# Kernel tuning notes

Measured on AMD Instinct MI355X. Metric: run time of the kernel, lower is better.

## Reference

```python
import jax, jax.numpy as jnp
import numpy as np

R = 4          # corr_radius
SLOPE = 0.1    # leaky relu negative slope


def _conv(x, w, b, pad):
    y = jax.lax.conv_general_dilated(
        x, w, window_strides=(1, 1), padding=[(pad, pad), (pad, pad)],
        dimension_numbers=("NCHW", "OIHW", "NCHW"))
    return y + b[None, :, None, None]


def _correlation(x1, x2):
    # Fused windowed cost volume: cv[b, i*(2R+1)+j, h, w] = mean_c x1[b,c,h,w] * x2[b,c,h+i-R,w+j-R]
    B, C, H, W = x1.shape
    x2p = jnp.pad(x2, ((0, 0), (0, 0), (R, R), (R, R)))
    cv = jnp.stack(
        [jnp.mean(x1 * jax.lax.dynamic_slice(x2p, (0, 0, i, j), (B, C, H, W)), axis=1)
         for i in range(2 * R + 1) for j in range(2 * R + 1)], axis=1)
    return cv  # (B, (2R+1)^2, H, W)


def setup_inputs() -> dict:
    key = jax.random.key(0)
    ks = jax.random.split(key, 20)
    B, H, W = 2, 256, 256
    pyr = 24
    inp = {
        "feat0": jax.random.normal(ks[0], (B, 2 * pyr, H, W), jnp.float32),
        "feat1": jax.random.normal(ks[1], (B, 2 * pyr, H, W), jnp.float32),
        "last_feat": jax.random.normal(ks[2], (B, 64, H, W), jnp.float32),
        "last_flow": jax.random.normal(ks[3], (B, 4, H, W), jnp.float32),
    }
    in_ch = (2 * R + 1) ** 2 + 2 * (2 * pyr) + 64 + 4  # 245
    dims = [(160, in_ch, 1), (128, 160, 3), (112, 128, 3), (96, 112, 3), (64, 96, 3), (4, 64, 3)]
    for n, (co, ci, k) in enumerate(dims, 1):
        scale = 1.0 / np.sqrt(ci * k * k)
        inp[f"w{n}"] = jax.random.normal(ks[4 + 2 * n], (co, ci, k, k), jnp.float32) * scale
        inp[f"b{n}"] = jnp.zeros((co,), jnp.float32)
    return inp


def reference(feat0, feat1, last_feat, last_flow,
              w1, b1, w2, b2, w3, b3, w4, b4, w5, b5, w6, b6):
    lrelu = lambda x: jax.nn.leaky_relu(x, SLOPE)
    volume = lrelu(_correlation(feat0, feat1))
    feat = jnp.concatenate([volume, feat0, feat1, last_feat, last_flow], axis=1)
    x = lrelu(_conv(feat, w1, b1, 0))   # 1x1 conv
    x = lrelu(_conv(x, w2, b2, 1))
    x = lrelu(_conv(x, w3, b3, 1))
    x = lrelu(_conv(x, w4, b4, 1))
    x = lrelu(_conv(x, w5, b5, 1))
    flow = _conv(x, w6, b6, 1)          # final ConvBlock, act=None
    return flow, x
```

## Files before the change

kernel.cpp:

```cpp
#include <hip/hip_runtime.h>
#include <cstdint>
#include <cstddef>


using short8 = __attribute__((ext_vector_type(8))) short;
using f32x4  = __attribute__((ext_vector_type(4))) float;
typedef unsigned short u16;

__device__ __forceinline__ u16 rne_bf16(float f) {
  unsigned u = __float_as_uint(f);
  u += 0x7FFFu + ((u >> 16) & 1u);
  return (u16)(u >> 16);
}

__device__ __forceinline__ void mfma16(const short8& a, const short8& b, f32x4& c) {
  asm("v_mfma_f32_16x16x32_bf16 %0, %1, %2, %0" : "+v"(c) : "v"(a), "v"(b));
}

__device__ __forceinline__ unsigned pk_f16(float a, float b) {
  unsigned r;
  asm("v_cvt_pkrtz_f16_f32 %0, %1, %2" : "=v"(r) : "v"(a), "v"(b));
  return r;
}

__device__ __forceinline__ void dot2(float& acc, unsigned a, unsigned b) {
  asm("v_dot2_f32_f16 %0, %1, %2, %0" : "+v"(acc) : "v"(a), "v"(b));
}

__device__ __forceinline__ void gload16(const void* g, void* l) {
  __builtin_amdgcn_global_load_lds(
      (const __attribute__((address_space(1))) unsigned int*)g,
      (__attribute__((address_space(3))) unsigned int*)l, 16, 0, 0);
}

__global__ __launch_bounds__(256) void prep1_kernel(const float* __restrict__ w1,
                                                    u16* __restrict__ w1p) {
  int idx = blockIdx.x * 256 + threadIdx.x;
  int co = idx >> 8, cip = idx & 255;
  float v = 0.f;
  if (co < 160 && cip < 245) {
    int ci = (cip < 164) ? (cip + 81) : (cip - 164);
    v = w1[co * 245 + ci];
  }
  w1p[idx] = rne_bf16(v);
}

template<int CO, int CIr, int BM, int APLN, int CIP>
__global__ __launch_bounds__(256) void prep3s_kernel(const float* __restrict__ w,
                                                     u16* __restrict__ wp) {
  int idx = blockIdx.x * 256 + threadIdx.x;
  int ci = idx % CIP; int rest = idx / CIP;
  int row = rest % APLN; int dyp = rest / APLN;
  int dx = row / BM, co = row % BM;
  float v = 0.f;
  if (dx < 3 && co < CO && ci < CIr)
    v = w[(co * CIr + ci) * 9 + dyp * 3 + dx];
  wp[idx] = rne_bf16(v);
}

template<int CO, int CI, int COP, int CIP>
__global__ __launch_bounds__(256) void prep3_kernel(const float* __restrict__ w,
                                                    u16* __restrict__ wp) {
  int idx = blockIdx.x * 256 + threadIdx.x;
  int ci = idx % CIP; int rest = idx / CIP;
  int co = rest % COP; int tap = rest / COP;
  float v = 0.f;
  if (co < CO && ci < CI) v = w[(co * CI + ci) * 9 + tap];
  wp[idx] = rne_bf16(v);
}

__global__ __launch_bounds__(256) void prep_bias_kernel(const float* __restrict__ b1,
    const float* __restrict__ b2, const float* __restrict__ b3,
    const float* __restrict__ b4, const float* __restrict__ b5,
    float* __restrict__ bp, u16* __restrict__ zbuf) {
  int i = blockIdx.x * 256 + threadIdx.x;
  if (i < 128) zbuf[i] = 0;
  float v = 0.f;
  if (i < 160) v = b1[i];
  else if (i < 288) v = b2[i - 160];
  else if (i < 416) { int c = i - 288; v = (c < 112) ? b3[c] : 0.f; }
  else if (i < 512) v = b4[i - 416];
  else if (i < 576) v = b5[i - 512];
  else return;
  bp[i] = v;
}

template<int NDY>
__device__ __forceinline__ void corr_compute(const uint2* __restrict__ win_s,
                                             const unsigned* __restrict__ f0p,
                                             float* __restrict__ cv,
                                             int row, int col, int dy0) {
#pragma unroll
  for (int d = 0; d < NDY; ++d) {
    const int r = row + dy0 + d;
#pragma unroll
    for (int cpp = 0; cpp < 6; ++cpp) {
      const uint2* base = win_s + (cpp * 10 + r) * 72 + col;
#pragma unroll
      for (int dx = 0; dx < 9; ++dx) {
        const uint2 v = base[dx];
        dot2(cv[d * 9 + dx], v.x, f0p[2 * cpp]);
        dot2(cv[d * 9 + dx], v.y, f0p[2 * cpp + 1]);
      }
    }
  }
}

__global__ __launch_bounds__(256) void corr2_kernel(const float* __restrict__ f0,
                                                    const float* __restrict__ f1,
                                                    u16* __restrict__ X1) {
  __shared__ uint2 win_s[4320];
  const int bid = blockIdx.x;
  const int swz = (bid & 7) * 128 + (bid >> 3);
  const int b = swz >> 9, rest = swz & 511;
  const int hp = rest >> 2, ct = rest & 3;
  const int h0 = hp << 1, w0 = ct << 6;
  const int tid = threadIdx.x, lane = tid & 63, wv = tid >> 6;
  const int half = wv >> 1, row = wv & 1, col = lane;

  float cv[45];
#pragma unroll
  for (int t = 0; t < 45; ++t) cv[t] = 0.f;

#pragma unroll 1
  for (int cc = 0; cc < 2; ++cc) {
    if (cc) __syncthreads();
    unsigned f0p[12];
    {
      const float* p0 = f0 + (((size_t)(b * 48 + cc * 24)) << 16)
                           + ((h0 + row) << 8) + (w0 + col);
#pragma unroll
      for (int j = 0; j < 12; ++j)
        f0p[j] = pk_f16(p0[(2 * j) << 16], p0[(2 * j + 1) << 16]);
    }
#pragma unroll 1
    for (int i = tid; i < 4320; i += 256) {
      const int c = i % 72;
      const int q = i / 72;
      const int r = q % 10;
      const int cpp = q / 10;
      const int hin = h0 + r - 4, win = w0 + c - 4;
      float v0 = 0.f, v1 = 0.f, v2 = 0.f, v3 = 0.f;
      if ((unsigned)hin < 256u && (unsigned)win < 256u) {
        const float* p = f1 + (((size_t)(b * 48 + cc * 24 + cpp * 4)) << 16)
                            + (hin << 8) + win;
        v0 = p[0]; v1 = p[1 << 16]; v2 = p[2 << 16]; v3 = p[3 << 16];
      }
      win_s[i] = make_uint2(pk_f16(v0, v1), pk_f16(v2, v3));
    }
    __syncthreads();
    if (half == 0) corr_compute<4>(win_s, f0p, cv, row, col, 0);
    else           corr_compute<5>(win_s, f0p, cv, row, col, 4);
  }

  const size_t pix = ((size_t)b << 16) + ((size_t)(h0 + row) << 8) + (w0 + col);
  u16* dst = X1 + pix * 256;
  const float sc = 1.0f / 48.0f;
  if (half == 0) {
#pragma unroll
    for (int qq = 0; qq < 9; ++qq) {
      u16 e[4];
#pragma unroll
      for (int j = 0; j < 4; ++j) {
        float v = cv[qq * 4 + j] * sc;
        v = v > 0.f ? v : 0.1f * v;
        e[j] = rne_bf16(v);
      }
      uint2 u;
      u.x = (unsigned)e[0] | ((unsigned)e[1] << 16);
      u.y = (unsigned)e[2] | ((unsigned)e[3] << 16);
      *(uint2*)(dst + 164 + qq * 4) = u;
    }
  } else {
#pragma unroll
    for (int qq = 0; qq < 14; ++qq) {
      u16 e[4];
#pragma unroll
      for (int j = 0; j < 4; ++j) {
        int t = qq * 4 + j;
        float v = 0.f;
        if (t < 45) {
          v = cv[t] * sc;
          v = v > 0.f ? v : 0.1f * v;
        }
        e[j] = rne_bf16(v);
      }
      uint2 u;
      u.x = (unsigned)e[0] | ((unsigned)e[1] << 16);
      u.y = (unsigned)e[2] | ((unsigned)e[3] << 16);
      *(uint2*)(dst + 200 + qq * 4) = u;
    }
  }
}

__global__ __launch_bounds__(256) void concat_kernel(const float* __restrict__ f0,
                                                     const float* __restrict__ f1,
                                                     const float* __restrict__ lf,
                                                     const float* __restrict__ lfl,
                                                     u16* __restrict__ X1) {
  __shared__ float s[16][68];
  const int t = threadIdx.x;
  const size_t px0 = (size_t)blockIdx.x * 64;
  const int b = blockIdx.x >> 10;
  const int hw0 = (blockIdx.x & 1023) * 64;

#pragma unroll 1
  for (int cc = 0; cc < 11; ++cc) {
    __syncthreads();
    {
      int px = t & 63, cg = t >> 6;
#pragma unroll
      for (int r = 0; r < 4; ++r) {
        int cl = cg * 4 + r;
        int c = cc * 16 + cl;
        int hw = hw0 + px;
        float v = 0.f;
        if (c < 48)       v = f0[(((size_t)(b * 48 + c)) << 16) + hw];
        else if (c < 96)  v = f1[(((size_t)(b * 48 + (c - 48))) << 16) + hw];
        else if (c < 160) v = lf[(((size_t)(b * 64 + (c - 96))) << 16) + hw];
        else if (c < 164) v = lfl[(((size_t)(b * 4 + (c - 160))) << 16) + hw];
        s[cl][px] = v;
      }
    }
    __syncthreads();
    {
      int px = t >> 2, g = t & 3;
      int cbase = cc * 16 + g * 4;
      if (cbase < 164) {
        ushort4 u;
        u.x = rne_bf16(s[g * 4 + 0][px]);
        u.y = rne_bf16(s[g * 4 + 1][px]);
        u.z = rne_bf16(s[g * 4 + 2][px]);
        u.w = rne_bf16(s[g * 4 + 3][px]);
        *(ushort4*)(X1 + (px0 + px) * 256 + cbase) = u;
      }
    }
  }
}

template<int CI, int BM, int APLN, int KS, int OSTRIDE, bool LRELU, bool OBF, int COF32>
__global__ __launch_bounds__(256) void convs_kernel(const u16* __restrict__ Xin,
    const u16* __restrict__ Wp, const float* __restrict__ bias,
    const u16* __restrict__ zbuf, u16* __restrict__ Xout,
    float* __restrict__ outF) {
  constexpr int NCH = CI / 32;
  constexpr int NDX = (KS == 3) ? 3 : 1;
  constexpr int AROUNDS = APLN / 64;
  constexpr int BROUNDS = (KS == 3) ? 3 : 2;
  constexpr int MF = BM / 32;
  constexpr int AELEMS = AROUNDS * 2048;
  constexpr int BPXMAX = (KS == 3) ? 132 : 128;
  __shared__ u16 lds[(AROUNDS + BROUNDS) * 2048];

  const int tid = threadIdx.x;
  const int lane = tid & 63, wv = tid >> 6;
  const int wm = wv >> 1, wn = wv & 1;
  const int bid = blockIdx.x;
  const int swz = (bid & 7) * 128 + (bid >> 3);
  const int bi = swz >> 9;
  const int h = (swz >> 1) & 255;
  const int w0 = (swz & 1) << 7;
  const int l15 = lane & 15, segr = lane >> 4;

  size_t aofs[AROUNDS];
#pragma unroll
  for (int r = 0; r < AROUNDS; ++r) {
    int slot = r * 256 + tid;
    int row = slot >> 2, sp = slot & 3;
    int seg = sp ^ ((row >> 1) & 3);
    aofs[r] = (size_t)row * CI + seg * 8;
  }
  size_t bofs[BROUNDS];
  bool bcolv[BROUNDS];
#pragma unroll
  for (int r = 0; r < BROUNDS; ++r) {
    int slot = r * 256 + tid;
    int pxl = slot >> 2, sp = slot & 3;
    int seg = sp ^ ((pxl >> 1) & 3);
    int px = (KS == 3) ? (w0 + pxl - 2) : (w0 + pxl);
    bcolv[r] = ((unsigned)px < 256u) && (pxl < BPXMAX);
    bofs[r] = (size_t)px * CI + seg * 8;
  }

  f32x4 acc[MF][4];
  const f32x4 zf = {0.f, 0.f, 0.f, 0.f};
#pragma unroll
  for (int m = 0; m < MF; ++m)
#pragma unroll
    for (int n = 0; n < 4; ++n) acc[m][n] = zf;

  int dy = 0, c = 0;
#pragma unroll 1
  for (int ph = 0; ph < NDX * NCH; ++ph) {
    __syncthreads();
    const u16* Wph = Wp + ((size_t)dy * APLN) * CI + c * 32;
#pragma unroll
    for (int r = 0; r < AROUNDS; ++r)
      gload16(Wph + aofs[r], &lds[r * 2048 + wv * 512]);
    const int hin = (KS == 3) ? (h + dy - 1) : h;
    const bool rv = (unsigned)hin < 256u;
    const u16* Brow = Xin + ((size_t)((bi << 8) + (rv ? hin : 0)) << 8) * CI + c * 32;
#pragma unroll
    for (int r = 0; r < BROUNDS; ++r) {
      const u16* src = (rv && bcolv[r]) ? (Brow + bofs[r]) : zbuf;
      gload16(src, &lds[AELEMS + r * 2048 + wv * 512]);
    }
    __syncthreads();

#pragma unroll
    for (int dx = 0; dx < NDX; ++dx) {
      short8 bfr[4];
#pragma unroll
      for (int n = 0; n < 4; ++n) {
        int p = wn * 64 + n * 16 + l15;
        int pxl = (KS == 3) ? (p + dx + 1) : p;
        int ba = (AELEMS * 2) + pxl * 64 + ((segr ^ ((pxl >> 1) & 3)) << 4);
        bfr[n] = *(const short8*)((const char*)lds + ba);
      }
      short8 afr[MF];
#pragma unroll
      for (int m = 0; m < MF; ++m) {
        int row = dx * BM + wm * (BM / 2) + m * 16 + l15;
        int aa = row * 64 + ((segr ^ ((row >> 1) & 3)) << 4);
        afr[m] = *(const short8*)((const char*)lds + aa);
      }
#pragma unroll
      for (int m = 0; m < MF; ++m)
#pragma unroll
        for (int n = 0; n < 4; ++n) mfma16(afr[m], bfr[n], acc[m][n]);
    }
    if (++c == NCH) { c = 0; ++dy; }
  }
  asm volatile("s_nop 7\n\ts_nop 7");

  const int co_sub = (lane >> 4) << 2;
  const size_t pixbase = ((size_t)((bi << 8) + h)) << 8;
#pragma unroll
  for (int m = 0; m < MF; ++m) {
    const int co = wm * (BM / 2) + m * 16 + co_sub;
#pragma unroll
    for (int n = 0; n < 4; ++n) {
      const int px = w0 + wn * 64 + n * 16 + l15;
      f32x4 v = acc[m][n];
      float t[4];
#pragma unroll
      for (int r = 0; r < 4; ++r) {
        float x = v[r] + bias[co + r];
        if (LRELU) x = x > 0.f ? x : 0.1f * x;
        t[r] = x;
      }
      if (OBF) {
        ushort4 u;
        u.x = rne_bf16(t[0]); u.y = rne_bf16(t[1]);
        u.z = rne_bf16(t[2]); u.w = rne_bf16(t[3]);
        *(ushort4*)(Xout + (pixbase + px) * OSTRIDE + co) = u;
      }
      if (COF32 > 0) {
#pragma unroll
        for (int r = 0; r < 4; ++r) {
          int cch = co + r;
          if (cch < COF32)
            outF[(((size_t)bi * COF32 + cch) << 16) + (h << 8) + px] = t[r];
        }
      }
    }
  }
}

template<int CI, int COP, int MF, int KS, bool LRELU, bool OBF, int COF32>
__global__ __launch_bounds__(256) void conv_kernel(const u16* __restrict__ Xin,
                                                   const u16* __restrict__ Wp,
                                                   const float* __restrict__ bias,
                                                   u16* __restrict__ Xout, int ostride,
                                                   float* __restrict__ outF) {
  const int lane = threadIdx.x & 63, wv = threadIdx.x >> 6;
  const int bi = blockIdx.x >> 9;
  const int h = (blockIdx.x >> 1) & 255;
  const int w0 = (blockIdx.x & 1) << 7;
  const int co0 = blockIdx.y * (MF * 16);
  const int l15 = lane & 15, klane = (lane >> 4) << 3;
  const int ncol0 = w0 + wv * 32 + l15;
  const int rowbase = (bi << 8) + h;

  const f32x4 zf = {0.f, 0.f, 0.f, 0.f};
  const short8 z8 = {0, 0, 0, 0, 0, 0, 0, 0};
  f32x4 acc[MF][2];
#pragma unroll
  for (int m = 0; m < MF; ++m) { acc[m][0] = zf; acc[m][1] = zf; }

#pragma unroll 1
  for (int chunk = 0; chunk < CI / 32; ++chunk) {
#pragma unroll
    for (int tap = 0; tap < KS * KS; ++tap) {
      const int dy = (KS == 3) ? tap / 3 - 1 : 0;
      const int dx = (KS == 3) ? tap % 3 - 1 : 0;
      const int hin = h + dy;
      if (KS == 3 && (unsigned)hin >= 256u) continue;
      short8 bf[2];
#pragma unroll
      for (int nf = 0; nf < 2; ++nf) {
        int win = ncol0 + nf * 16 + dx;
        short8 v = z8;
        if (KS == 1 || (unsigned)win < 256u)
          v = *(const short8*)(Xin + ((size_t)(((bi << 8) + hin) * 256 + win)) * CI
                               + chunk * 32 + klane);
        bf[nf] = v;
      }
#pragma unroll
      for (int m = 0; m < MF; ++m) {
        const short8 af = *(const short8*)(Wp + ((size_t)(tap * COP + co0 + m * 16 + l15)) * CI
                                           + chunk * 32 + klane);
        mfma16(af, bf[0], acc[m][0]);
        mfma16(af, bf[1], acc[m][1]);
      }
    }
  }
  asm volatile("s_nop 7\n\ts_nop 7");

  const int co_sub = (lane >> 4) << 2;
  const size_t pixrow = (size_t)rowbase << 8;
#pragma unroll
  for (int m = 0; m < MF; ++m) {
    const int co = co0 + m * 16 + co_sub;
#pragma unroll
    for (int nf = 0; nf < 2; ++nf) {
      const int w = ncol0 + nf * 16;
      f32x4 v = acc[m][nf];
      if constexpr (OBF) {
        float t[4];
#pragma unroll
        for (int r = 0; r < 4; ++r) {
          float x = v[r] + bias[co + r];
          if constexpr (LRELU) x = x > 0.f ? x : 0.1f * x;
          t[r] = x;
        }
        ushort4 u;
        u.x = rne_bf16(t[0]); u.y = rne_bf16(t[1]);
        u.z = rne_bf16(t[2]); u.w = rne_bf16(t[3]);
        *(ushort4*)(Xout + (pixrow + w) * (size_t)ostride + co) = u;
      }
      if constexpr (COF32 > 0) {
#pragma unroll
        for (int r = 0; r < 4; ++r) {
          int c = co + r;
          if (c < COF32) {
            float x = v[r] + bias[c];
            if constexpr (LRELU) x = x > 0.f ? x : 0.1f * x;
            outF[((((size_t)bi * COF32) + c) << 16) + (h << 8) + w] = x;
          }
        }
      }
    }
  }
}

extern "C" void kernel_launch(void* const* d_in, const int* in_sizes, int n_in,
                              void* d_out, int out_size, void* d_ws, size_t ws_size,
                              hipStream_t stream) {
  const float* feat0 = (const float*)d_in[0];
  const float* feat1 = (const float*)d_in[1];
  const float* lfeat = (const float*)d_in[2];
  const float* lflow = (const float*)d_in[3];
  const float* w1 = (const float*)d_in[4];  const float* b1 = (const float*)d_in[5];
  const float* w2 = (const float*)d_in[6];  const float* b2 = (const float*)d_in[7];
  const float* w3 = (const float*)d_in[8];  const float* b3 = (const float*)d_in[9];
  const float* w4 = (const float*)d_in[10]; const float* b4 = (const float*)d_in[11];
  const float* w5 = (const float*)d_in[12]; const float* b5 = (const float*)d_in[13];
  const float* w6 = (const float*)d_in[14]; const float* b6 = (const float*)d_in[15];

  u16* ws = (u16*)d_ws;
  u16* X1 = ws;
  u16* X2 = ws + 33554432;
  u16* X3 = ws;
  u16* X4 = ws + 33554432;
  u16* X5 = ws;
  u16* X6 = ws + 33554432;
  u16* w1p = ws + 54525952;
  u16* w2p = w1p + 49152;
  u16* w3p = w2p + 184320;
  u16* w4p = w3p + 147456;
  u16* w5p = w4p + 147456;
  u16* w6p = w5p + 55296;
  float* bp = (float*)(w6p + 9216);
  u16* zbuf = (u16*)(bp + 576);

  const float* bp1 = bp;
  const float* bp2 = bp + 160;
  const float* bp3 = bp + 288;
  const float* bp4 = bp + 416;
  const float* bp5 = bp + 512;

  float* flow = (float*)d_out;
  float* xout = (float*)d_out + 524288;

  prep1_kernel<<<192, 256, 0, stream>>>(w1, w1p);
  prep3s_kernel<128, 160, 128, 384, 160><<<720, 256, 0, stream>>>(w2, w2p);
  prep3s_kernel<112, 128, 128, 384, 128><<<576, 256, 0, stream>>>(w3, w3p);
  prep3s_kernel< 96, 112,  96, 320, 128><<<480, 256, 0, stream>>>(w4, w4p);
  prep3s_kernel< 64,  96,  64, 192,  96><<<216, 256, 0, stream>>>(w5, w5p);
  prep3_kernel<  4,  64,  16,  64><<< 36, 256, 0, stream>>>(w6, w6p);
  prep_bias_kernel<<<3, 256, 0, stream>>>(b1, b2, b3, b4, b5, bp, zbuf);

  corr2_kernel<<<1024, 256, 0, stream>>>(feat0, feat1, X1);
  concat_kernel<<<2048, 256, 0, stream>>>(feat0, feat1, lfeat, lflow, X1);

  convs_kernel<256, 160, 192, 1, 160, true, true,  0><<<1024, 256, 0, stream>>>(X1, w1p, bp1, zbuf, X2, nullptr);
  convs_kernel<160, 128, 384, 3, 128, true, true,  0><<<1024, 256, 0, stream>>>(X2, w2p, bp2, zbuf, X3, nullptr);
  convs_kernel<128, 128, 384, 3, 128, true, true,  0><<<1024, 256, 0, stream>>>(X3, w3p, bp3, zbuf, X4, nullptr);
  convs_kernel<128,  96, 320, 3,  96, true, true,  0><<<1024, 256, 0, stream>>>(X4, w4p, bp4, zbuf, X5, nullptr);
  convs_kernel< 96,  64, 192, 3,  64, true, true, 64><<<1024, 256, 0, stream>>>(X5, w5p, bp5, zbuf, X6, xout);
  conv_kernel< 64,  16, 1, 3, false, false, 4><<<dim3(1024, 1), 256, 0, stream>>>(X6, w6p, b6, nullptr, 0, flow);
}
```

Before: 330.2 us.

## Double-buffer correlation window loads and fuse feat0/feat1 bf16 concat into corr

The correlation kernel now processes channels in four chunks of 12 with double-buffered shared-memory windows, prefetching the next chunk's feat1/feat0 values into registers while computing the current one. It also writes the bf16 copies of feat0 and feat1 (the latter taken from the center of the shared window) directly into the concat buffer. This lets the concat kernel handle only last_feat and last_flow, avoiding a second global read of feat0/feat1. The cost is higher register pressure (prefetch arrays) and feat1 passing through an fp16 round-trip before bf16 conversion, which could slightly change rounding.

Result: faster. 303.1 us (-8.2%).

```diff
diff --git a/kernel.cpp b/kernel.cpp
--- a/kernel.cpp
+++ b/kernel.cpp
@@ -1,4 +1,5 @@
 #include <hip/hip_runtime.h>
+#include <hip/hip_fp16.h>
 #include <cstdint>
 #include <cstddef>
 
@@ -86,16 +87,16 @@
 }
 
 template<int NDY>
-__device__ __forceinline__ void corr_compute(const uint2* __restrict__ win_s,
-                                             const unsigned* __restrict__ f0p,
-                                             float* __restrict__ cv,
-                                             int row, int col, int dy0) {
+__device__ __forceinline__ void corr_compute3(const uint2* __restrict__ wb,
+                                              const unsigned* __restrict__ f0p,
+                                              float* __restrict__ cv,
+                                              int row, int col, int dy0) {
 #pragma unroll
   for (int d = 0; d < NDY; ++d) {
     const int r = row + dy0 + d;
 #pragma unroll
-    for (int cpp = 0; cpp < 6; ++cpp) {
-      const uint2* base = win_s + (cpp * 10 + r) * 72 + col;
+    for (int cpp = 0; cpp < 3; ++cpp) {
+      const uint2* base = wb + (cpp * 10 + r) * 72 + col;
 #pragma unroll
       for (int dx = 0; dx < 9; ++dx) {
         const uint2 v = base[dx];
@@ -106,10 +107,10 @@
   }
 }
 
-__global__ __launch_bounds__(256) void corr2_kernel(const float* __restrict__ f0,
+__global__ __launch_bounds__(256) void corr3_kernel(const float* __restrict__ f0,
                                                     const float* __restrict__ f1,
                                                     u16* __restrict__ X1) {
-  __shared__ uint2 win_s[4320];
+  __shared__ uint2 win_s[2][2160];
   const int bid = blockIdx.x;
   const int swz = (bid & 7) * 128 + (bid >> 3);
   const int b = swz >> 9, rest = swz & 511;
@@ -118,42 +119,91 @@
   const int tid = threadIdx.x, lane = tid & 63, wv = tid >> 6;
   const int half = wv >> 1, row = wv & 1, col = lane;
 
+  int slot_off[9];
+  unsigned ok_mask = 0;
+#pragma unroll
+  for (int k = 0; k < 9; ++k) {
+    int i = k * 256 + tid;
+    bool act = i < 2160;
+    int ii = act ? i : 0;
+    int c = ii % 72, q = ii / 72;
+    int r = q % 10, cpp = q / 10;
+    int hin = h0 + r - 4, win = w0 + c - 4;
+    bool ok = act && ((unsigned)hin < 256u) && ((unsigned)win < 256u);
+    if (ok) ok_mask |= (1u << k);
+    slot_off[k] = ((b * 48 + cpp * 4) << 16) + (hin << 8) + win;
+  }
+  const int pixoff = ((b * 48) << 16) + ((h0 + row) << 8) + (w0 + col);
+  const size_t pix = ((size_t)b << 16) + ((size_t)(h0 + row) << 8) + (w0 + col);
+
+  float sv[9][4];
+  float f0v[12];
+#pragma unroll
+  for (int k = 0; k < 9; ++k)
+#pragma unroll
+    for (int j = 0; j < 4; ++j) sv[k][j] = 0.f;
+
+  auto issue = [&](int cc) {
+#pragma unroll
+    for (int k = 0; k < 9; ++k) {
+      if (ok_mask & (1u << k)) {
+        const float* p = f1 + (size_t)(slot_off[k] + ((cc * 12) << 16));
+#pragma unroll
+        for (int j = 0; j < 4; ++j) sv[k][j] = p[(size_t)j << 16];
+      }
+    }
+#pragma unroll
+    for (int j = 0; j < 12; ++j)
+      f0v[j] = f0[(size_t)(pixoff + ((cc * 12 + j) << 16))];
+  };
+
   float cv[45];
 #pragma unroll
   for (int t = 0; t < 45; ++t) cv[t] = 0.f;
 
+  issue(0);
+  int buf = 0;
 #pragma unroll 1
-  for (int cc = 0; cc < 2; ++cc) {
-    if (cc) __syncthreads();
-    unsigned f0p[12];
+  for (int cc = 0; cc < 4; ++cc) {
+    unsigned f0p[6];
+#pragma unroll
+    for (int j = 0; j < 6; ++j) f0p[j] = pk_f16(f0v[2 * j], f0v[2 * j + 1]);
     {
-      const float* p0 = f0 + (((size_t)(b * 48 + cc * 24)) << 16)
-                           + ((h0 + row) << 8) + (w0 + col);
-#pragma unroll
-      for (int j = 0; j < 12; ++j)
-        f0p[j] = pk_f16(p0[(2 * j) << 16], p0[(2 * j + 1) << 16]);
-    }
-#pragma unroll 1
-    for (int i = tid; i < 4320; i += 256) {
-      const int c = i % 72;
-      const int q = i / 72;
-      const int r = q % 10;
-      const int cpp = q / 10;
-      const int hin = h0 + r - 4, win = w0 + c - 4;
-      float v0 = 0.f, v1 = 0.f, v2 = 0.f, v3 = 0.f;
-      if ((unsigned)hin < 256u && (unsigned)win < 256u) {
-        const float* p = f1 + (((size_t)(b * 48 + cc * 24 + cpp * 4)) << 16)
-                            + (hin << 8) + win;
-        v0 = p[0]; v1 = p[1 << 16]; v2 = p[2 << 16]; v3 = p[3 << 16];
-      }
-      win_s[i] = make_uint2(pk_f16(v0, v1), pk_f16(v2, v3));
-    }
+      u16* dst0 = X1 + pix * 256 + cc * 12;
+#pragma unroll
+      for (int q = 0; q < 3; ++q) {
+        uint2 u;
+        u.x = (unsigned)rne_bf16(f0v[4 * q + 0]) | ((unsigned)rne_bf16(f0v[4 * q + 1]) << 16);
+        u.y = (unsigned)rne_bf16(f0v[4 * q + 2]) | ((unsigned)rne_bf16(f0v[4 * q + 3]) << 16);
+        *(uint2*)(dst0 + 4 * q) = u;
+      }
+    }
+    uint2* wb = &win_s[buf][0];
+#pragma unroll
+    for (int k = 0; k < 9; ++k)
+      if (k * 256 + tid < 2160)
+        wb[k * 256 + tid] = make_uint2(pk_f16(sv[k][0], sv[k][1]),
+                                       pk_f16(sv[k][2], sv[k][3]));
     __syncthreads();
-    if (half == 0) corr_compute<4>(win_s, f0p, cv, row, col, 0);
-    else           corr_compute<5>(win_s, f0p, cv, row, col, 4);
-  }
-
-  const size_t pix = ((size_t)b << 16) + ((size_t)(h0 + row) << 8) + (w0 + col);
+    if (cc < 3) issue(cc + 1);
+    {
+      const uint2* own = wb + (row + 4) * 72 + (col + 4);
+      u16* dst1 = X1 + pix * 256 + 48 + cc * 12;
+#pragma unroll
+      for (int q = 0; q < 3; ++q) {
+        uint2 v = own[q * 720];
+        __half2 lo = *(__half2*)&v.x, hi = *(__half2*)&v.y;
+        uint2 u;
+        u.x = (unsigned)rne_bf16(__half2float(lo.x)) | ((unsigned)rne_bf16(__half2float(lo.y)) << 16);
+        u.y = (unsigned)rne_bf16(__half2float(hi.x)) | ((unsigned)rne_bf16(__half2float(hi.y)) << 16);
+        *(uint2*)(dst1 + 4 * q) = u;
+      }
+    }
+    if (half == 0) corr_compute3<4>(wb, f0p, cv, row, col, 0);
+    else           corr_compute3<5>(wb, f0p, cv, row, col, 4);
+    buf ^= 1;
+  }
+
   u16* dst = X1 + pix * 256;
   const float sc = 1.0f / 48.0f;
   if (half == 0) {
@@ -193,11 +243,9 @@
   }
 }
 
-__global__ __launch_bounds__(256) void concat_kernel(const float* __restrict__ f0,
-                                                     const float* __restrict__ f1,
-                                                     const float* __restrict__ lf,
-                                                     const float* __restrict__ lfl,
-                                                     u16* __restrict__ X1) {
+__global__ __launch_bounds__(256) void concat68_kernel(const float* __restrict__ lf,
+                                                       const float* __restrict__ lfl,
+                                                       u16* __restrict__ X1) {
   __shared__ float s[16][68];
   const int t = threadIdx.x;
   const size_t px0 = (size_t)blockIdx.x * 64;
@@ -205,7 +253,7 @@
   const int hw0 = (blockIdx.x & 1023) * 64;
 
 #pragma unroll 1
-  for (int cc = 0; cc < 11; ++cc) {
+  for (int cc = 0; cc < 5; ++cc) {
     __syncthreads();
     {
       int px = t & 63, cg = t >> 6;
@@ -215,10 +263,8 @@
         int c = cc * 16 + cl;
         int hw = hw0 + px;
         float v = 0.f;
-        if (c < 48)       v = f0[(((size_t)(b * 48 + c)) << 16) + hw];
-        else if (c < 96)  v = f1[(((size_t)(b * 48 + (c - 48))) << 16) + hw];
-        else if (c < 160) v = lf[(((size_t)(b * 64 + (c - 96))) << 16) + hw];
-        else if (c < 164) v = lfl[(((size_t)(b * 4 + (c - 160))) << 16) + hw];
+        if (c < 64)       v = lf[(((size_t)(b * 64 + c)) << 16) + hw];
+        else if (c < 68)  v = lfl[(((size_t)(b * 4 + (c - 64))) << 16) + hw];
         s[cl][px] = v;
       }
     }
@@ -226,13 +272,13 @@
     {
       int px = t >> 2, g = t & 3;
       int cbase = cc * 16 + g * 4;
-      if (cbase < 164) {
+      if (cbase < 68) {
         ushort4 u;
         u.x = rne_bf16(s[g * 4 + 0][px]);
         u.y = rne_bf16(s[g * 4 + 1][px]);
         u.z = rne_bf16(s[g * 4 + 2][px]);
         u.w = rne_bf16(s[g * 4 + 3][px]);
-        *(ushort4*)(X1 + (px0 + px) * 256 + cbase) = u;
+        *(ushort4*)(X1 + (px0 + px) * 256 + 96 + cbase) = u;
       }
     }
   }
@@ -501,8 +547,8 @@
   prep3_kernel<  4,  64,  16,  64><<< 36, 256, 0, stream>>>(w6, w6p);
   prep_bias_kernel<<<3, 256, 0, stream>>>(b1, b2, b3, b4, b5, bp, zbuf);
 
-  corr2_kernel<<<1024, 256, 0, stream>>>(feat0, feat1, X1);
-  concat_kernel<<<2048, 256, 0, stream>>>(feat0, feat1, lfeat, lflow, X1);
+  corr3_kernel<<<1024, 256, 0, stream>>>(feat0, feat1, X1);
+  concat68_kernel<<<2048, 256, 0, stream>>>(lfeat, lflow, X1);
 
   convs_kernel<256, 160, 192, 1, 160, true, true,  0><<<1024, 256, 0, stream>>>(X1, w1p, bp1, zbuf, X2, nullptr);
   convs_kernel<160, 128, 384, 3, 128, true, true,  0><<<1024, 256, 0, stream>>>(X2, w2p, bp2, zbuf, X3, nullptr);
```

## Pre-pack features to fp16 quads and double-buffer correlation window via global_load_lds

Applied to the files above, without the earlier changes.

The concat kernel now writes feat0/feat1 as channel-quad-packed fp16 buffers in addition to the other bf16 channels. A new correlation kernel streams the f1 window into double-buffered LDS with async global_load_lds and reads f0 from the packed buffer. It also writes the bf16 feat0/feat1 channels of X1 itself. This cuts strided fp32 gathers and overlaps window loads with the dot2 compute, at the cost of an extra intermediate buffer write and read plus an fp16-to-bf16 double rounding of the feature channels.

Result: faster. 312.8 us (-5.3%).

```diff
diff --git a/kernel.cpp b/kernel.cpp
--- a/kernel.cpp
+++ b/kernel.cpp
@@ -1,4 +1,5 @@
 #include <hip/hip_runtime.h>
+#include <hip/hip_fp16.h>
 #include <cstdint>
 #include <cstddef>
 
@@ -31,6 +32,14 @@
   __builtin_amdgcn_global_load_lds(
       (const __attribute__((address_space(1))) unsigned int*)g,
       (__attribute__((address_space(3))) unsigned int*)l, 16, 0, 0);
+}
+
+__device__ __forceinline__ uint2 quad_to_bf16(uint2 v) {
+  __half2 lo = *(__half2*)&v.x, hi = *(__half2*)&v.y;
+  uint2 u;
+  u.x = (unsigned)rne_bf16(__half2float(lo.x)) | ((unsigned)rne_bf16(__half2float(lo.y)) << 16);
+  u.y = (unsigned)rne_bf16(__half2float(hi.x)) | ((unsigned)rne_bf16(__half2float(hi.y)) << 16);
+  return u;
 }
 
 __global__ __launch_bounds__(256) void prep1_kernel(const float* __restrict__ w1,
@@ -85,119 +94,10 @@
   bp[i] = v;
 }
 
-template<int NDY>
-__device__ __forceinline__ void corr_compute(const uint2* __restrict__ win_s,
-                                             const unsigned* __restrict__ f0p,
-                                             float* __restrict__ cv,
-                                             int row, int col, int dy0) {
-#pragma unroll
-  for (int d = 0; d < NDY; ++d) {
-    const int r = row + dy0 + d;
-#pragma unroll
-    for (int cpp = 0; cpp < 6; ++cpp) {
-      const uint2* base = win_s + (cpp * 10 + r) * 72 + col;
-#pragma unroll
-      for (int dx = 0; dx < 9; ++dx) {
-        const uint2 v = base[dx];
-        dot2(cv[d * 9 + dx], v.x, f0p[2 * cpp]);
-        dot2(cv[d * 9 + dx], v.y, f0p[2 * cpp + 1]);
-      }
-    }
-  }
-}
-
-__global__ __launch_bounds__(256) void corr2_kernel(const float* __restrict__ f0,
-                                                    const float* __restrict__ f1,
-                                                    u16* __restrict__ X1) {
-  __shared__ uint2 win_s[4320];
-  const int bid = blockIdx.x;
-  const int swz = (bid & 7) * 128 + (bid >> 3);
-  const int b = swz >> 9, rest = swz & 511;
-  const int hp = rest >> 2, ct = rest & 3;
-  const int h0 = hp << 1, w0 = ct << 6;
-  const int tid = threadIdx.x, lane = tid & 63, wv = tid >> 6;
-  const int half = wv >> 1, row = wv & 1, col = lane;
-
-  float cv[45];
-#pragma unroll
-  for (int t = 0; t < 45; ++t) cv[t] = 0.f;
-
-#pragma unroll 1
-  for (int cc = 0; cc < 2; ++cc) {
-    if (cc) __syncthreads();
-    unsigned f0p[12];
-    {
-      const float* p0 = f0 + (((size_t)(b * 48 + cc * 24)) << 16)
-                           + ((h0 + row) << 8) + (w0 + col);
-#pragma unroll
-      for (int j = 0; j < 12; ++j)
-        f0p[j] = pk_f16(p0[(2 * j) << 16], p0[(2 * j + 1) << 16]);
-    }
-#pragma unroll 1
-    for (int i = tid; i < 4320; i += 256) {
-      const int c = i % 72;
-      const int q = i / 72;
-      const int r = q % 10;
-      const int cpp = q / 10;
-      const int hin = h0 + r - 4, win = w0 + c - 4;
-      float v0 = 0.f, v1 = 0.f, v2 = 0.f, v3 = 0.f;
-      if ((unsigned)hin < 256u && (unsigned)win < 256u) {
-        const float* p = f1 + (((size_t)(b * 48 + cc * 24 + cpp * 4)) << 16)
-                            + (hin << 8) + win;
-        v0 = p[0]; v1 = p[1 << 16]; v2 = p[2 << 16]; v3 = p[3 << 16];
-      }
-      win_s[i] = make_uint2(pk_f16(v0, v1), pk_f16(v2, v3));
-    }
-    __syncthreads();
-    if (half == 0) corr_compute<4>(win_s, f0p, cv, row, col, 0);
-    else           corr_compute<5>(win_s, f0p, cv, row, col, 4);
-  }
-
-  const size_t pix = ((size_t)b << 16) + ((size_t)(h0 + row) << 8) + (w0 + col);
-  u16* dst = X1 + pix * 256;
-  const float sc = 1.0f / 48.0f;
-  if (half == 0) {
-#pragma unroll
-    for (int qq = 0; qq < 9; ++qq) {
-      u16 e[4];
-#pragma unroll
-      for (int j = 0; j < 4; ++j) {
-        float v = cv[qq * 4 + j] * sc;
-        v = v > 0.f ? v : 0.1f * v;
-        e[j] = rne_bf16(v);
-      }
-      uint2 u;
-      u.x = (unsigned)e[0] | ((unsigned)e[1] << 16);
-      u.y = (unsigned)e[2] | ((unsigned)e[3] << 16);
-      *(uint2*)(dst + 164 + qq * 4) = u;
-    }
-  } else {
-#pragma unroll
-    for (int qq = 0; qq < 14; ++qq) {
-      u16 e[4];
-#pragma unroll
-      for (int j = 0; j < 4; ++j) {
-        int t = qq * 4 + j;
-        float v = 0.f;
-        if (t < 45) {
-          v = cv[t] * sc;
-          v = v > 0.f ? v : 0.1f * v;
-        }
-        e[j] = rne_bf16(v);
-      }
-      uint2 u;
-      u.x = (unsigned)e[0] | ((unsigned)e[1] << 16);
-      u.y = (unsigned)e[2] | ((unsigned)e[3] << 16);
-      *(uint2*)(dst + 200 + qq * 4) = u;
-    }
-  }
-}
-
-__global__ __launch_bounds__(256) void concat_kernel(const float* __restrict__ f0,
-                                                     const float* __restrict__ f1,
-                                                     const float* __restrict__ lf,
-                                                     const float* __restrict__ lfl,
-                                                     u16* __restrict__ X1) {
+__global__ __launch_bounds__(256) void concat_all_kernel(const float* __restrict__ f0,
+    const float* __restrict__ f1, const float* __restrict__ lf,
+    const float* __restrict__ lfl, u16* __restrict__ X1,
+    u16* __restrict__ f0q, u16* __restrict__ f1q) {
   __shared__ float s[16][68];
   const int t = threadIdx.x;
   const size_t px0 = (size_t)blockIdx.x * 64;
@@ -226,7 +126,15 @@
     {
       int px = t >> 2, g = t & 3;
       int cbase = cc * 16 + g * 4;
-      if (cbase < 164) {
+      if (cbase < 96) {
+        int qq = cbase >> 2;
+        u16* dq = (qq < 12) ? (f0q + ((size_t)((b * 12 + qq) << 16) << 2))
+                            : (f1q + ((size_t)((b * 12 + qq - 12) << 16) << 2));
+        uint2 u;
+        u.x = pk_f16(s[g * 4 + 0][px], s[g * 4 + 1][px]);
+        u.y = pk_f16(s[g * 4 + 2][px], s[g * 4 + 3][px]);
+        *(uint2*)(dq + (size_t)(hw0 + px) * 4) = u;
+      } else if (cbase < 164) {
         ushort4 u;
         u.x = rne_bf16(s[g * 4 + 0][px]);
         u.y = rne_bf16(s[g * 4 + 1][px]);
@@ -234,6 +142,141 @@
         u.w = rne_bf16(s[g * 4 + 3][px]);
         *(ushort4*)(X1 + (px0 + px) * 256 + cbase) = u;
       }
+    }
+  }
+}
+
+template<int NDY>
+__device__ __forceinline__ void corr_acc(const uint2* __restrict__ wb,
+                                         const unsigned* __restrict__ f0p,
+                                         float* __restrict__ cv,
+                                         int row, int col, int dy0) {
+#pragma unroll
+  for (int d = 0; d < NDY; ++d) {
+    const int r = row + dy0 + d;
+#pragma unroll
+    for (int q = 0; q < 3; ++q) {
+      const uint2* base = wb + (q * 10 + r) * 80 + (col + 4);
+#pragma unroll
+      for (int dx = 0; dx < 9; ++dx) {
+        const uint2 v = base[dx];
+        dot2(cv[d * 9 + dx], v.x, f0p[2 * q]);
+        dot2(cv[d * 9 + dx], v.y, f0p[2 * q + 1]);
+      }
+    }
+  }
+}
+
+__global__ __launch_bounds__(256, 4) void corr5_kernel(const u16* __restrict__ f0q,
+                                                       const u16* __restrict__ f1q,
+                                                       const u16* __restrict__ zbuf,
+                                                       u16* __restrict__ X1) {
+  __shared__ char wlds[2][20480];
+  const int bid = blockIdx.x;
+  const int swz = (bid & 7) * 128 + (bid >> 3);
+  const int b = swz >> 9, rest = swz & 511;
+  const int hp = rest >> 2, ct = rest & 3;
+  const int h0 = hp << 1, w0 = ct << 6;
+  const int tid = threadIdx.x, lane = tid & 63, wv = tid >> 6;
+  const int half = wv >> 1, row = wv & 1, col = lane;
+  const int pixhw = ((h0 + row) << 8) + (w0 + col);
+  const size_t pix = ((size_t)b << 16) + pixhw;
+
+  const u16* srcp[5];
+  bool okf[5];
+#pragma unroll
+  for (int ru = 0; ru < 5; ++ru) {
+    int u = ru * 256 + tid;
+    int uq = u / 400;
+    int rem = u - uq * 400;
+    int r = rem / 40, cu = rem - r * 40;
+    int hin = h0 + r - 4;
+    int wpx = w0 - 8 + 2 * cu;
+    bool ok = (u < 1200) && ((unsigned)hin < 256u) && ((unsigned)wpx < 256u);
+    okf[ru] = ok;
+    srcp[ru] = ok ? (f1q + (((size_t)((b * 12 + uq) << 16) + (hin << 8) + wpx) << 2))
+                  : zbuf;
+  }
+
+  float cv[45];
+#pragma unroll
+  for (int t = 0; t < 45; ++t) cv[t] = 0.f;
+
+#pragma unroll
+  for (int ru = 0; ru < 5; ++ru)
+    gload16(srcp[ru], &wlds[0][ru * 4096 + wv * 1024]);
+
+#pragma unroll 1
+  for (int cc = 0; cc < 4; ++cc) {
+    __syncthreads();
+    if (cc < 3) {
+#pragma unroll
+      for (int ru = 0; ru < 5; ++ru) {
+        const u16* s = okf[ru] ? (srcp[ru] + (size_t)(cc + 1) * 786432) : zbuf;
+        gload16(s, &wlds[(cc + 1) & 1][ru * 4096 + wv * 1024]);
+      }
+    }
+    const uint2* wb = (const uint2*)&wlds[cc & 1][0];
+
+    const u16* f0base = f0q + (((size_t)((b * 12 + cc * 3) << 16) + pixhw) << 2);
+    uint2 q0 = *(const uint2*)(f0base);
+    uint2 q1 = *(const uint2*)(f0base + 262144);
+    uint2 q2 = *(const uint2*)(f0base + 524288);
+    unsigned f0p[6] = {q0.x, q0.y, q1.x, q1.y, q2.x, q2.y};
+
+    {
+      u16* dst0 = X1 + pix * 256 + cc * 12;
+      *(uint2*)(dst0)     = quad_to_bf16(q0);
+      *(uint2*)(dst0 + 4) = quad_to_bf16(q1);
+      *(uint2*)(dst0 + 8) = quad_to_bf16(q2);
+    }
+    {
+      u16* dst1 = X1 + pix * 256 + 48 + cc * 12;
+#pragma unroll
+      for (int q = 0; q < 3; ++q) {
+        uint2 v = wb[(q * 10 + row + 4) * 80 + (col + 8)];
+        *(uint2*)(dst1 + 4 * q) = quad_to_bf16(v);
+      }
+    }
+    if (half == 0) corr_acc<4>(wb, f0p, cv, row, col, 0);
+    else           corr_acc<5>(wb, f0p, cv, row, col, 4);
+  }
+
+  u16* dst = X1 + pix * 256;
+  const float sc = 1.0f / 48.0f;
+  if (half == 0) {
+#pragma unroll
+    for (int qq = 0; qq < 9; ++qq) {
+      u16 e[4];
+#pragma unroll
+      for (int j = 0; j < 4; ++j) {
+        float v = cv[qq * 4 + j] * sc;
+        v = v > 0.f ? v : 0.1f * v;
+        e[j] = rne_bf16(v);
+      }
+      uint2 u;
+      u.x = (unsigned)e[0] | ((unsigned)e[1] << 16);
+      u.y = (unsigned)e[2] | ((unsigned)e[3] << 16);
+      *(uint2*)(dst + 164 + qq * 4) = u;
+    }
+  } else {
+#pragma unroll
+    for (int qq = 0; qq < 14; ++qq) {
+      u16 e[4];
+#pragma unroll
+      for (int j = 0; j < 4; ++j) {
+        int t = qq * 4 + j;
+        float v = 0.f;
+        if (t < 45) {
+          v = cv[t] * sc;
+          v = v > 0.f ? v : 0.1f * v;
+        }
+        e[j] = rne_bf16(v);
+      }
+      uint2 u;
+      u.x = (unsigned)e[0] | ((unsigned)e[1] << 16);
+      u.y = (unsigned)e[2] | ((unsigned)e[3] << 16);
+      *(uint2*)(dst + 200 + qq * 4) = u;
     }
   }
 }
@@ -475,6 +518,8 @@
   u16* X4 = ws + 33554432;
   u16* X5 = ws;
   u16* X6 = ws + 33554432;
+  u16* f0q = ws + 33554432;
+  u16* f1q = ws + 39845888;
   u16* w1p = ws + 54525952;
   u16* w2p = w1p + 49152;
   u16* w3p = w2p + 184320;
@@ -501,8 +546,8 @@
   prep3_kernel<  4,  64,  16,  64><<< 36, 256, 0, stream>>>(w6, w6p);
   prep_bias_kernel<<<3, 256, 0, stream>>>(b1, b2, b3, b4, b5, bp, zbuf);
 
-  corr2_kernel<<<1024, 256, 0, stream>>>(feat0, feat1, X1);
-  concat_kernel<<<2048, 256, 0, stream>>>(feat0, feat1, lfeat, lflow, X1);
+  concat_all_kernel<<<2048, 256, 0, stream>>>(feat0, feat1, lfeat, lflow, X1, f0q, f1q);
+  corr5_kernel<<<1024, 256, 0, stream>>>(f0q, f1q, zbuf, X1);
 
   convs_kernel<256, 160, 192, 1, 160, true, true,  0><<<1024, 256, 0, stream>>>(X1, w1p, bp1, zbuf, X2, nullptr);
   convs_kernel<160, 128, 384, 3, 128, true, true,  0><<<1024, 256, 0, stream>>>(X2, w2p, bp2, zbuf, X3, nullptr);
```
